# Kernel tuning notes

Hardware: AMD Instinct MI355X
Metric: run time of the kernel (lower is better)

Reference implementation:

```python
import jax, jax.numpy as jnp
import numpy as np

N_NODES = 100000


def gcn_conv(x, W, b, src, dst, n):
    # PyG GCNConv: add self-loops, symmetric deg^{-1/2} normalization,
    # h = x @ W, out[i] = sum_j norm_ij * h[j] + b
    loop = jnp.arange(n, dtype=src.dtype)
    s = jnp.concatenate([src, loop])
    d = jnp.concatenate([dst, loop])
    h = x @ W  # [N, F_out]
    deg = jax.ops.segment_sum(jnp.ones_like(d, dtype=x.dtype), d, num_segments=n)
    dinv = jnp.where(deg > 0, jax.lax.rsqrt(deg), 0.0)
    norm = dinv[s] * dinv[d]  # [E+N]
    msgs = h[s] * norm[:, None]  # gather + scale
    out = jax.ops.segment_sum(msgs, d, num_segments=n)  # scatter-add
    return out + b


def setup_inputs() -> dict:
    key = jax.random.key(0)
    ks = jax.random.split(key, 8)
    n, e = N_NODES, 1600000
    return {
        "clinical": jax.random.normal(ks[0], (n, 64), dtype=jnp.float32),
        "mel": jax.random.normal(ks[1], (n, 1024), dtype=jnp.float32),
        "edge_index": jax.random.randint(ks[2], (2, e), 0, n, dtype=jnp.int64),
        "W_mel": jax.random.normal(ks[3], (1024, 128), dtype=jnp.float32) * 0.03,
        "b_mel": jnp.zeros((128,), dtype=jnp.float32),
        "W_cat": jax.random.normal(ks[4], (192, 128), dtype=jnp.float32) * 0.07,
        "b_cat": jnp.zeros((128,), dtype=jnp.float32),
        "W1": jax.random.normal(ks[5], (128, 128), dtype=jnp.float32) * 0.09,
        "b1": jnp.zeros((128,), dtype=jnp.float32),
        "W2": jax.random.normal(ks[6], (128, 4), dtype=jnp.float32) * 0.09,
        "b2": jnp.zeros((4,), dtype=jnp.float32),
    }


def reference(clinical, mel, edge_index, W_mel, b_mel, W_cat, b_cat, W1, b1, W2, b2):
    n = clinical.shape[0]
    src, dst = edge_index[0], edge_index[1]
    m = jax.nn.relu(mel @ W_mel + b_mel)            # [N, 128]
    x = jnp.concatenate([clinical, m], axis=1)       # [N, 192]
    x = jax.nn.relu(x @ W_cat + b_cat)               # [N, 128]
    x = jax.nn.relu(gcn_conv(x, W1, b1, src, dst, n))
    x = gcn_conv(x, W2, b2, src, dst, n)             # [N, 4]
    return x
```

## Files before the change

### kernel.cpp

```cpp
#include <hip/hip_runtime.h>
#include <cstdint>


typedef short short4_t __attribute__((ext_vector_type(4)));
typedef short short8_t __attribute__((ext_vector_type(8)));
typedef float floatx4 __attribute__((ext_vector_type(4)));

__device__ __forceinline__ short f2bf(float f) {
  union { float f; unsigned u; } v;
  v.f = f;
  unsigned r = v.u + 0x7fffu + ((v.u >> 16) & 1u);
  return (short)(r >> 16);
}

__device__ __forceinline__ bool detect_i64(const int* __restrict__ ei) {
  int nz = 0;
#pragma unroll
  for (int i = 1; i < 64; i += 2) nz |= ei[i];
  return nz == 0;
}
__device__ __forceinline__ int load_src(const int* __restrict__ ei, int e, bool is64) {
  return is64 ? ei[2 * e] : ei[e];
}
__device__ __forceinline__ int load_dst(const int* __restrict__ ei, int e, int E, bool is64) {
  return is64 ? ei[2 * (E + e)] : ei[E + e];
}

__global__ __launch_bounds__(256) void zero_int_k(int* __restrict__ p, int n) {
  int i = blockIdx.x * 256 + threadIdx.x;
  if (i < n) p[i] = 0;
}

__global__ __launch_bounds__(256) void count_deg_k(const int* __restrict__ ei,
                                                   int* __restrict__ degi, int E) {
  const bool is64 = detect_i64(ei);
  int e = blockIdx.x * 256 + threadIdx.x;
  if (e < E) atomicAdd(&degi[load_dst(ei, e, E, is64)], 1);
}

__global__ __launch_bounds__(256) void dinv_k(const int* __restrict__ degi,
                                              float* __restrict__ dinv, int n) {
  int i = blockIdx.x * 256 + threadIdx.x;
  if (i < n) dinv[i] = rsqrtf((float)degi[i] + 1.0f);
}

__global__ __launch_bounds__(256) void scan_reduce_k(const int* __restrict__ degi,
                                                     int* __restrict__ partial, int n) {
  __shared__ int s[256];
  int t = threadIdx.x;
  int i = blockIdx.x * 256 + t;
  s[t] = (i < n) ? degi[i] : 0;
  __syncthreads();
#pragma unroll
  for (int off = 128; off > 0; off >>= 1) {
    if (t < off) s[t] += s[t + off];
    __syncthreads();
  }
  if (t == 0) partial[blockIdx.x] = s[0];
}

__global__ __launch_bounds__(512) void scan_partials_k(const int* __restrict__ partial,
                                                       int* __restrict__ excl, int B,
                                                       int* __restrict__ rowptr, int n, int E) {
  __shared__ int s[512];
  int t = threadIdx.x;
  int v = (t < B) ? partial[t] : 0;
  s[t] = v;
  __syncthreads();
  for (int off = 1; off < 512; off <<= 1) {
    int x = (t >= off) ? s[t - off] : 0;
    __syncthreads();
    s[t] += x;
    __syncthreads();
  }
  if (t < B) excl[t] = s[t] - v;
  if (t == 0) rowptr[n] = E;
}

__global__ __launch_bounds__(256) void scan_final_k(const int* __restrict__ degi,
                                                    const int* __restrict__ excl,
                                                    int* __restrict__ rowptr, int n) {
  __shared__ int s[256];
  int t = threadIdx.x;
  int i = blockIdx.x * 256 + t;
  int v = (i < n) ? degi[i] : 0;
  s[t] = v;
  __syncthreads();
  for (int off = 1; off < 256; off <<= 1) {
    int x = (t >= off) ? s[t - off] : 0;
    __syncthreads();
    s[t] += x;
    __syncthreads();
  }
  if (i < n) rowptr[i] = excl[blockIdx.x] + s[t] - v;
}

__global__ __launch_bounds__(256) void fill_col_k(const int* __restrict__ ei,
                                                  const int* __restrict__ rowptr,
                                                  int* __restrict__ fill,
                                                  int* __restrict__ col, int E) {
  const bool is64 = detect_i64(ei);
  int e = blockIdx.x * 256 + threadIdx.x;
  if (e < E) {
    int s = load_src(ei, e, is64);
    int d = load_dst(ei, e, E, is64);
    int pos = rowptr[d] + atomicAdd(&fill[d], 1);
    col[pos] = s;
  }
}

__global__ __launch_bounds__(256) void convW_k(const float* __restrict__ W,
                                               short* __restrict__ Wt) {
  int idx = blockIdx.x * 256 + threadIdx.x;
  int nn = idx >> 10;
  int k = idx & 1023;
  Wt[idx] = f2bf(W[(size_t)k * 128 + nn]);
}

__global__ __launch_bounds__(256) void mel_gemm_mfma_k(const float* __restrict__ A,
                                                       const short* __restrict__ Wt,
                                                       const float* __restrict__ bias,
                                                       float* __restrict__ C, int n) {
  __shared__ short Asm[128][72];
  __shared__ short Bsm[128][72];
  const int tid = threadIdx.x;
  const int row0 = blockIdx.x * 128;
  const int lane = tid & 63;
  const int wv = tid >> 6;
  const int quad = lane >> 4;
  const int cbase = lane & 15;

  floatx4 acc[2][8];
#pragma unroll
  for (int tr = 0; tr < 2; ++tr)
#pragma unroll
    for (int tc = 0; tc < 8; ++tc) acc[tr][tc] = (floatx4){0.f, 0.f, 0.f, 0.f};

  for (int kc = 0; kc < 16; ++kc) {
    __syncthreads();
#pragma unroll
    for (int j = 0; j < 8; ++j) {
      int idx = j * 256 + tid;
      int row = idx >> 4, c4 = idx & 15;
      int grow = row0 + row;
      floatx4 v = (floatx4){0.f, 0.f, 0.f, 0.f};
      if (grow < n) v = *(const floatx4*)(A + (size_t)grow * 1024 + kc * 64 + c4 * 4);
      short4_t s4;
      s4[0] = f2bf(v[0]); s4[1] = f2bf(v[1]); s4[2] = f2bf(v[2]); s4[3] = f2bf(v[3]);
      *(short4_t*)&Asm[row][c4 * 4] = s4;
    }
#pragma unroll
    for (int j = 0; j < 8; ++j) {
      int idx = j * 256 + tid;
      int nr = idx >> 4, c4 = idx & 15;
      *(short4_t*)&Bsm[nr][c4 * 4] =
          *(const short4_t*)(Wt + (size_t)nr * 1024 + kc * 64 + c4 * 4);
    }
    __syncthreads();
#pragma unroll
    for (int kk = 0; kk < 2; ++kk) {
      short8_t af[2], bf[8];
#pragma unroll
      for (int tr = 0; tr < 2; ++tr)
        af[tr] = *(const short8_t*)&Asm[wv * 32 + tr * 16 + cbase][kk * 32 + quad * 8];
#pragma unroll
      for (int tc = 0; tc < 8; ++tc)
        bf[tc] = *(const short8_t*)&Bsm[tc * 16 + cbase][kk * 32 + quad * 8];
#pragma unroll
      for (int tr = 0; tr < 2; ++tr)
#pragma unroll
        for (int tc = 0; tc < 8; ++tc)
          acc[tr][tc] = __builtin_amdgcn_mfma_f32_16x16x32_bf16(af[tr], bf[tc],
                                                                acc[tr][tc], 0, 0, 0);
    }
  }
  float bb[8];
#pragma unroll
  for (int tc = 0; tc < 8; ++tc) bb[tc] = bias[tc * 16 + cbase];
#pragma unroll
  for (int tr = 0; tr < 2; ++tr) {
#pragma unroll
    for (int r = 0; r < 4; ++r) {
      int grow = row0 + wv * 32 + tr * 16 + quad * 4 + r;
      if (grow < n) {
#pragma unroll
        for (int tc = 0; tc < 8; ++tc) {
          float v = acc[tr][tc][r] + bb[tc];
          C[(size_t)grow * 128 + tc * 16 + cbase] = fmaxf(v, 0.f);
        }
      }
    }
  }
}

template <bool RELU, bool HASBIAS>
__global__ __launch_bounds__(256) void gemm128_k(const float* __restrict__ A, int K,
                                                 const float* __restrict__ B,
                                                 const float* __restrict__ bias,
                                                 float* __restrict__ C, int n) {
  __shared__ float As[64][33];
  __shared__ float4 Bs[32][32];
  const int tid = threadIdx.x;
  const int tx = tid & 31, ty = tid >> 5;
  const int row0 = blockIdx.x * 64;
  float acc[8][4];
#pragma unroll
  for (int i = 0; i < 8; ++i)
#pragma unroll
    for (int j = 0; j < 4; ++j) acc[i][j] = 0.f;

  const int nChunks = K >> 5;
  for (int kc = 0; kc < nChunks; ++kc) {
    __syncthreads();
#pragma unroll
    for (int j = 0; j < 2; ++j) {
      int idx = tid + j * 256;
      int ar = idx >> 3, ac4 = idx & 7;
      int grow = row0 + ar;
      float4 v = make_float4(0.f, 0.f, 0.f, 0.f);
      if (grow < n) v = *(const float4*)(A + (size_t)grow * K + kc * 32 + ac4 * 4);
      As[ar][ac4 * 4 + 0] = v.x;
      As[ar][ac4 * 4 + 1] = v.y;
      As[ar][ac4 * 4 + 2] = v.z;
      As[ar][ac4 * 4 + 3] = v.w;
    }
#pragma unroll
    for (int j = 0; j < 4; ++j) {
      int idx = tid + j * 256;
      int br = idx >> 5, bc4 = idx & 31;
      Bs[br][bc4] = *(const float4*)(B + (size_t)(kc * 32 + br) * 128 + bc4 * 4);
    }
    __syncthreads();
#pragma unroll
    for (int kk = 0; kk < 32; ++kk) {
      float4 b = Bs[kk][tx];
#pragma unroll
      for (int i = 0; i < 8; ++i) {
        float a = As[ty * 8 + i][kk];
        acc[i][0] += a * b.x;
        acc[i][1] += a * b.y;
        acc[i][2] += a * b.z;
        acc[i][3] += a * b.w;
      }
    }
  }
  float4 bb = make_float4(0.f, 0.f, 0.f, 0.f);
  if (HASBIAS) bb = *(const float4*)(bias + tx * 4);
#pragma unroll
  for (int i = 0; i < 8; ++i) {
    int grow = row0 + ty * 8 + i;
    if (grow < n) {
      float4 o;
      o.x = acc[i][0] + bb.x;
      o.y = acc[i][1] + bb.y;
      o.z = acc[i][2] + bb.z;
      o.w = acc[i][3] + bb.w;
      if (RELU) {
        o.x = fmaxf(o.x, 0.f);
        o.y = fmaxf(o.y, 0.f);
        o.z = fmaxf(o.z, 0.f);
        o.w = fmaxf(o.w, 0.f);
      }
      *(float4*)(C + (size_t)grow * 128 + tx * 4) = o;
    }
  }
}

__global__ __launch_bounds__(256) void gemm_cat_k(const float* __restrict__ A1,
                                                  const float* __restrict__ A2,
                                                  const float* __restrict__ B,
                                                  const float* __restrict__ bias,
                                                  float* __restrict__ C, int n) {
  __shared__ float As[64][33];
  __shared__ float4 Bs[32][32];
  const int tid = threadIdx.x;
  const int tx = tid & 31, ty = tid >> 5;
  const int row0 = blockIdx.x * 64;
  float acc[8][4];
#pragma unroll
  for (int i = 0; i < 8; ++i)
#pragma unroll
    for (int j = 0; j < 4; ++j) acc[i][j] = 0.f;

  for (int kc = 0; kc < 6; ++kc) {
    __syncthreads();
#pragma unroll
    for (int j = 0; j < 2; ++j) {
      int idx = tid + j * 256;
      int ar = idx >> 3, ac4 = idx & 7;
      int grow = row0 + ar;
      int kcol = kc * 32 + ac4 * 4;
      float4 v = make_float4(0.f, 0.f, 0.f, 0.f);
      if (grow < n) {
        v = (kcol < 64) ? *(const float4*)(A1 + (size_t)grow * 64 + kcol)
                        : *(const float4*)(A2 + (size_t)grow * 128 + (kcol - 64));
      }
      As[ar][ac4 * 4 + 0] = v.x;
      As[ar][ac4 * 4 + 1] = v.y;
      As[ar][ac4 * 4 + 2] = v.z;
      As[ar][ac4 * 4 + 3] = v.w;
    }
#pragma unroll
    for (int j = 0; j < 4; ++j) {
      int idx = tid + j * 256;
      int br = idx >> 5, bc4 = idx & 31;
      Bs[br][bc4] = *(const float4*)(B + (size_t)(kc * 32 + br) * 128 + bc4 * 4);
    }
    __syncthreads();
#pragma unroll
    for (int kk = 0; kk < 32; ++kk) {
      float4 b = Bs[kk][tx];
#pragma unroll
      for (int i = 0; i < 8; ++i) {
        float a = As[ty * 8 + i][kk];
        acc[i][0] += a * b.x;
        acc[i][1] += a * b.y;
        acc[i][2] += a * b.z;
        acc[i][3] += a * b.w;
      }
    }
  }
  float4 bb = *(const float4*)(bias + tx * 4);
#pragma unroll
  for (int i = 0; i < 8; ++i) {
    int grow = row0 + ty * 8 + i;
    if (grow < n) {
      float4 o;
      o.x = fmaxf(acc[i][0] + bb.x, 0.f);
      o.y = fmaxf(acc[i][1] + bb.y, 0.f);
      o.z = fmaxf(acc[i][2] + bb.z, 0.f);
      o.w = fmaxf(acc[i][3] + bb.w, 0.f);
      *(float4*)(C + (size_t)grow * 128 + tx * 4) = o;
    }
  }
}

template <bool RELU>
__global__ __launch_bounds__(256) void gather128_k(const int* __restrict__ col,
                                                   const int* __restrict__ rowptr,
                                                   const float* __restrict__ dinv,
                                                   const float* __restrict__ h,
                                                   const float* __restrict__ bias,
                                                   float* __restrict__ out, int n) {
  const int node = blockIdx.x * 2 + (threadIdx.x >> 7);
  const int f = threadIdx.x & 127;
  if (node >= n) return;
  const int beg = rowptr[node], end = rowptr[node + 1];
  float acc = 0.f;
  int p = beg;
  for (; p + 4 <= end; p += 4) {
    int s0 = col[p], s1 = col[p + 1], s2 = col[p + 2], s3 = col[p + 3];
    float d0 = dinv[s0], d1 = dinv[s1], d2 = dinv[s2], d3 = dinv[s3];
    float h0 = h[(size_t)s0 * 128 + f];
    float h1 = h[(size_t)s1 * 128 + f];
    float h2 = h[(size_t)s2 * 128 + f];
    float h3 = h[(size_t)s3 * 128 + f];
    acc += d0 * h0 + d1 * h1 + d2 * h2 + d3 * h3;
  }
  for (; p < end; ++p) {
    int s = col[p];
    acc += dinv[s] * h[(size_t)s * 128 + f];
  }
  const float di = dinv[node];
  float v = di * (acc + di * h[(size_t)node * 128 + f]) + bias[f];
  if (RELU) v = fmaxf(v, 0.f);
  out[(size_t)node * 128 + f] = v;
}

__global__ __launch_bounds__(256) void gemm_small4_k(const float* __restrict__ A,
                                                     const float* __restrict__ W,
                                                     float* __restrict__ Y, int n) {
  __shared__ float Ws[512];
  int tid = threadIdx.x;
  Ws[tid] = W[tid];
  Ws[tid + 256] = W[tid + 256];
  __syncthreads();
  int row = blockIdx.x * 256 + tid;
  if (row >= n) return;
  const float4* A4 = (const float4*)(A + (size_t)row * 128);
  float a0 = 0.f, a1 = 0.f, a2 = 0.f, a3 = 0.f;
#pragma unroll
  for (int k4 = 0; k4 < 32; ++k4) {
    float4 a = A4[k4];
    const float* w = &Ws[k4 * 16];
    a0 += a.x * w[0] + a.y * w[4] + a.z * w[8] + a.w * w[12];
    a1 += a.x * w[1] + a.y * w[5] + a.z * w[9] + a.w * w[13];
    a2 += a.x * w[2] + a.y * w[6] + a.z * w[10] + a.w * w[14];
    a3 += a.x * w[3] + a.y * w[7] + a.z * w[11] + a.w * w[15];
  }
  *(float4*)(Y + (size_t)row * 4) = make_float4(a0, a1, a2, a3);
}

__global__ __launch_bounds__(256) void gather4_k(const int* __restrict__ col,
                                                 const int* __restrict__ rowptr,
                                                 const float* __restrict__ dinv,
                                                 const float* __restrict__ y,
                                                 const float* __restrict__ b2,
                                                 float* __restrict__ out, int n) {
  int node = blockIdx.x * 256 + threadIdx.x;
  if (node >= n) return;
  const int beg = rowptr[node], end = rowptr[node + 1];
  float ax = 0.f, ay = 0.f, az = 0.f, aw = 0.f;
  int p = beg;
  for (; p + 2 <= end; p += 2) {
    int s0 = col[p], s1 = col[p + 1];
    float d0 = dinv[s0], d1 = dinv[s1];
    float4 y0 = *(const float4*)(y + (size_t)s0 * 4);
    float4 y1 = *(const float4*)(y + (size_t)s1 * 4);
    ax += d0 * y0.x + d1 * y1.x;
    ay += d0 * y0.y + d1 * y1.y;
    az += d0 * y0.z + d1 * y1.z;
    aw += d0 * y0.w + d1 * y1.w;
  }
  for (; p < end; ++p) {
    int s = col[p];
    float ds = dinv[s];
    float4 yv = *(const float4*)(y + (size_t)s * 4);
    ax += ds * yv.x;
    ay += ds * yv.y;
    az += ds * yv.z;
    aw += ds * yv.w;
  }
  const float di = dinv[node];
  float4 yd = *(const float4*)(y + (size_t)node * 4);
  float4 o;
  o.x = di * (ax + di * yd.x) + b2[0];
  o.y = di * (ay + di * yd.y) + b2[1];
  o.z = di * (az + di * yd.z) + b2[2];
  o.w = di * (aw + di * yd.w) + b2[3];
  *(float4*)(out + (size_t)node * 4) = o;
}

extern "C" void kernel_launch(void* const* d_in, const int* in_sizes, int n_in,
                              void* d_out, int out_size, void* d_ws, size_t ws_size,
                              hipStream_t stream) {
  const float* clinical = (const float*)d_in[0];
  const float* mel = (const float*)d_in[1];
  const int* ei = (const int*)d_in[2];
  const float* W_mel = (const float*)d_in[3];
  const float* b_mel = (const float*)d_in[4];
  const float* W_cat = (const float*)d_in[5];
  const float* b_cat = (const float*)d_in[6];
  const float* W1 = (const float*)d_in[7];
  const float* b1 = (const float*)d_in[8];
  const float* W2 = (const float*)d_in[9];
  const float* b2 = (const float*)d_in[10];
  float* out = (float*)d_out;

  const int N = in_sizes[0] / 64;
  const int E = in_sizes[2] / 2;
  const int B = (N + 255) / 256;

  float* bufA = (float*)d_ws;
  float* bufB = bufA + (size_t)N * 128;
  float* dinv = bufB + (size_t)N * 128;
  float* ybuf = dinv + N;
  int* degi = (int*)(ybuf + (size_t)N * 4);
  int* rowptr = degi + N;
  int* fill = rowptr + (N + 1);
  int* partial = fill + N;
  int* excl = partial + 512;
  int* col = excl + 512;
  short* Wt = (short*)(col + E);

  const dim3 blk(256);

  zero_int_k<<<(N + 255) / 256, blk, 0, stream>>>(degi, N);
  count_deg_k<<<(E + 255) / 256, blk, 0, stream>>>(ei, degi, E);
  dinv_k<<<B, blk, 0, stream>>>(degi, dinv, N);
  scan_reduce_k<<<B, blk, 0, stream>>>(degi, partial, N);
  scan_partials_k<<<1, 512, 0, stream>>>(partial, excl, B, rowptr, N, E);
  scan_final_k<<<B, blk, 0, stream>>>(degi, excl, rowptr, N);
  zero_int_k<<<B, blk, 0, stream>>>(fill, N);
  fill_col_k<<<(E + 255) / 256, blk, 0, stream>>>(ei, rowptr, fill, col, E);
  convW_k<<<512, blk, 0, stream>>>(W_mel, Wt);

  mel_gemm_mfma_k<<<(N + 127) / 128, blk, 0, stream>>>(mel, Wt, b_mel, bufA, N);
  gemm_cat_k<<<(N + 63) / 64, blk, 0, stream>>>(clinical, bufA, W_cat, b_cat, bufB, N);
  gemm128_k<false, false><<<(N + 63) / 64, blk, 0, stream>>>(bufB, 128, W1, nullptr, bufA, N);

  gather128_k<true><<<(N + 1) / 2, blk, 0, stream>>>(col, rowptr, dinv, bufA, b1, bufB, N);

  gemm_small4_k<<<(N + 255) / 256, blk, 0, stream>>>(bufB, W2, ybuf, N);

  gather4_k<<<(N + 255) / 256, blk, 0, stream>>>(col, rowptr, dinv, ybuf, b2, out, N);
}
```

Before: 1.172 ms.

## Load mel GEMM operands directly from global memory into MFMA fragments, bypassing LDS

Removes the shared-memory staging and both barriers from the mel GEMM. Each lane now loads its A rows (fp32, converted to bf16 in registers) and its B fragments straight from global memory into MFMA operands. Out-of-range rows are clamped to the last row rather than zero-filled; their results are still dropped by the store guard. This cuts LDS traffic and synchronisation, but the global loads become less coalesced and the B weights are re-read by every wave without on-chip sharing, leaning on the caches.

```diff
diff --git a/kernel.cpp b/kernel.cpp
--- a/kernel.cpp
+++ b/kernel.cpp
@@ -121,14 +121,20 @@
                                                        const short* __restrict__ Wt,
                                                        const float* __restrict__ bias,
                                                        float* __restrict__ C, int n) {
-  __shared__ short Asm[128][72];
-  __shared__ short Bsm[128][72];
   const int tid = threadIdx.x;
-  const int row0 = blockIdx.x * 128;
   const int lane = tid & 63;
   const int wv = tid >> 6;
   const int quad = lane >> 4;
   const int cbase = lane & 15;
+  const int row0 = blockIdx.x * 128;
+
+  int r0 = row0 + wv * 32 + cbase;
+  int r1 = r0 + 16;
+  if (r0 > n - 1) r0 = n - 1;
+  if (r1 > n - 1) r1 = n - 1;
+  const float* __restrict__ a0p = A + (size_t)r0 * 1024;
+  const float* __restrict__ a1p = A + (size_t)r1 * 1024;
+  const short* __restrict__ bp = Wt + (size_t)cbase * 1024;
 
   floatx4 acc[2][8];
 #pragma unroll
@@ -137,43 +143,30 @@
     for (int tc = 0; tc < 8; ++tc) acc[tr][tc] = (floatx4){0.f, 0.f, 0.f, 0.f};
 
   for (int kc = 0; kc < 16; ++kc) {
-    __syncthreads();
-#pragma unroll
-    for (int j = 0; j < 8; ++j) {
-      int idx = j * 256 + tid;
-      int row = idx >> 4, c4 = idx & 15;
-      int grow = row0 + row;
-      floatx4 v = (floatx4){0.f, 0.f, 0.f, 0.f};
-      if (grow < n) v = *(const floatx4*)(A + (size_t)grow * 1024 + kc * 64 + c4 * 4);
-      short4_t s4;
-      s4[0] = f2bf(v[0]); s4[1] = f2bf(v[1]); s4[2] = f2bf(v[2]); s4[3] = f2bf(v[3]);
-      *(short4_t*)&Asm[row][c4 * 4] = s4;
-    }
-#pragma unroll
-    for (int j = 0; j < 8; ++j) {
-      int idx = j * 256 + tid;
-      int nr = idx >> 4, c4 = idx & 15;
-      *(short4_t*)&Bsm[nr][c4 * 4] =
-          *(const short4_t*)(Wt + (size_t)nr * 1024 + kc * 64 + c4 * 4);
-    }
-    __syncthreads();
 #pragma unroll
     for (int kk = 0; kk < 2; ++kk) {
-      short8_t af[2], bf[8];
-#pragma unroll
-      for (int tr = 0; tr < 2; ++tr)
-        af[tr] = *(const short8_t*)&Asm[wv * 32 + tr * 16 + cbase][kk * 32 + quad * 8];
-#pragma unroll
-      for (int tc = 0; tc < 8; ++tc)
-        bf[tc] = *(const short8_t*)&Bsm[tc * 16 + cbase][kk * 32 + quad * 8];
-#pragma unroll
-      for (int tr = 0; tr < 2; ++tr)
-#pragma unroll
-        for (int tc = 0; tc < 8; ++tc)
-          acc[tr][tc] = __builtin_amdgcn_mfma_f32_16x16x32_bf16(af[tr], bf[tc],
-                                                                acc[tr][tc], 0, 0, 0);
-    }
-  }
+      const int kb = kc * 64 + kk * 32 + quad * 8;
+      floatx4 va00 = *(const floatx4*)(a0p + kb);
+      floatx4 va01 = *(const floatx4*)(a0p + kb + 4);
+      floatx4 va10 = *(const floatx4*)(a1p + kb);
+      floatx4 va11 = *(const floatx4*)(a1p + kb + 4);
+      short8_t af0, af1;
+#pragma unroll
+      for (int j = 0; j < 4; ++j) {
+        af0[j] = f2bf(va00[j]);
+        af0[j + 4] = f2bf(va01[j]);
+        af1[j] = f2bf(va10[j]);
+        af1[j + 4] = f2bf(va11[j]);
+      }
+#pragma unroll
+      for (int tc = 0; tc < 8; ++tc) {
+        short8_t bf = *(const short8_t*)(bp + (size_t)tc * 16384 + kb);
+        acc[0][tc] = __builtin_amdgcn_mfma_f32_16x16x32_bf16(af0, bf, acc[0][tc], 0, 0, 0);
+        acc[1][tc] = __builtin_amdgcn_mfma_f32_16x16x32_bf16(af1, bf, acc[1][tc], 0, 0, 0);
+      }
+    }
+  }
+
   float bb[8];
 #pragma unroll
   for (int tc = 0; tc < 8; ++tc) bb[tc] = bias[tc * 16 + cbase];
```

After: 1.133 ms. 1.03x faster.
